# Performance work log

Measured on AMD Instinct MI355X. Metric: run time of the kernel, lower is better.

## Reference

```python
import jax, jax.numpy as jnp
import numpy as np

N_NODES = 50000
D_IN = 64
HID = 64
OUT = 64
NEG_SLOPE = 0.2


def setup_inputs() -> dict:
    key = jax.random.key(0)
    ks = jax.random.split(key, 16)
    s = 1.0 / np.sqrt(D_IN)
    inp = {
        "x": jax.random.normal(ks[0], (N_NODES, D_IN), dtype=jnp.float32),
        "edge_index": jax.random.randint(ks[1], (2, 1200000), 0, N_NODES, dtype=jnp.int64),
        # conv1 (GATConv, heads=1): separate src/dst projections + attention vectors + bias
        "W1_src": jax.random.uniform(ks[2], (D_IN, HID), jnp.float32, -s, s),
        "W1_dst": jax.random.uniform(ks[3], (D_IN, HID), jnp.float32, -s, s),
        "att1_src": jax.random.uniform(ks[4], (HID,), jnp.float32, -s, s),
        "att1_dst": jax.random.uniform(ks[5], (HID,), jnp.float32, -s, s),
        "b1": jnp.zeros((HID,), jnp.float32),
        # lin1 residual
        "Wl1": jax.random.uniform(ks[6], (D_IN, HID), jnp.float32, -s, s),
        "bl1": jnp.zeros((HID,), jnp.float32),
        # conv2
        "W2_src": jax.random.uniform(ks[7], (HID, OUT), jnp.float32, -s, s),
        "W2_dst": jax.random.uniform(ks[8], (HID, OUT), jnp.float32, -s, s),
        "att2_src": jax.random.uniform(ks[9], (OUT,), jnp.float32, -s, s),
        "att2_dst": jax.random.uniform(ks[10], (OUT,), jnp.float32, -s, s),
        "b2": jnp.zeros((OUT,), jnp.float32),
        # lin2 residual
        "Wl2": jax.random.uniform(ks[11], (HID, OUT), jnp.float32, -s, s),
        "bl2": jnp.zeros((OUT,), jnp.float32),
    }
    return inp


def _gat_conv(x, W_src, W_dst, att_src, att_dst, bias, src, dst, n_nodes):
    # project nodes: [N, C]
    h_src = x @ W_src
    h_dst = x @ W_dst
    # per-node attention logits: [N]
    a_src = h_src @ att_src
    a_dst = h_dst @ att_dst
    # per-edge score, leaky relu (slope 0.2)
    e = a_src[src] + a_dst[dst]  # [E]
    e = jnp.where(e >= 0, e, NEG_SLOPE * e)
    # segment softmax over incoming edges of each dst node
    seg_max = jax.lax.stop_gradient(
        jax.ops.segment_max(e, dst, num_segments=n_nodes))  # [N]
    w = jnp.exp(e - seg_max[dst])  # [E]
    seg_sum = jax.ops.segment_sum(w, dst, num_segments=n_nodes)  # [N]
    alpha = w / seg_sum[dst]  # [E]
    # weighted scatter-add of gathered src features
    msg = h_src[src] * alpha[:, None]  # [E, C]
    out = jax.ops.segment_sum(msg, dst, num_segments=n_nodes)  # [N, C]
    return out + bias


def reference(x, edge_index, W1_src, W1_dst, att1_src, att1_dst, b1, Wl1, bl1,
              W2_src, W2_dst, att2_src, att2_dst, b2, Wl2, bl2):
    src, dst = edge_index[0], edge_index[1]
    n = x.shape[0]
    h = _gat_conv(x, W1_src, W1_dst, att1_src, att1_dst, b1, src, dst, n)
    h = jax.nn.relu(h + x @ Wl1 + bl1)
    o = _gat_conv(h, W2_src, W2_dst, att2_src, att2_dst, b2, src, dst, n)
    o = jax.nn.relu(o + h @ Wl2 + bl2)
    return o
```

## Files before the change

kernel.cpp:

```cpp
#include <hip/hip_runtime.h>
#include <hip/hip_fp16.h>

#define NEG 0.2f
#define BSHIFT 9
#define BNODES 512
#define ECAP 14336

__device__ __forceinline__ void agg_core(
    int beg, int end, float ad, int lane, int g, int l,
    const int* __restrict__ ssrc, const float* __restrict__ asrc,
    const float2* __restrict__ h8,
    float& a0, float& a1, float& a2, float& a3, float& sumw) {
    a0 = a1 = a2 = a3 = sumw = 0.f;
    while (beg < end) {
        int nb = min(64, end - beg);
        int s_l = 0; float w_l = 0.f;
        if (lane < nb) {
            s_l = ssrc[beg + lane];
            float e = asrc[s_l] + ad;
            e = (e >= 0.f) ? e : NEG * e;
            w_l = __expf(e);
        }
        int i = 0;
        for (; i + 15 < nb; i += 16) {
            int iA = i + g, iB = i + 4 + g, iC = i + 8 + g, iD = i + 12 + g;
            int   sA = __shfl(s_l, iA, 64), sB = __shfl(s_l, iB, 64);
            int   sC = __shfl(s_l, iC, 64), sD = __shfl(s_l, iD, 64);
            float wA = __shfl(w_l, iA, 64), wB = __shfl(w_l, iB, 64);
            float wC = __shfl(w_l, iC, 64), wD = __shfl(w_l, iD, 64);
            float2 rA = h8[(size_t)sA * 16 + l];
            float2 rB = h8[(size_t)sB * 16 + l];
            float2 rC = h8[(size_t)sC * 16 + l];
            float2 rD = h8[(size_t)sD * 16 + l];
            float2 fA0 = __half22float2(((const __half2*)&rA)[0]);
            float2 fA1 = __half22float2(((const __half2*)&rA)[1]);
            float2 fB0 = __half22float2(((const __half2*)&rB)[0]);
            float2 fB1 = __half22float2(((const __half2*)&rB)[1]);
            float2 fC0 = __half22float2(((const __half2*)&rC)[0]);
            float2 fC1 = __half22float2(((const __half2*)&rC)[1]);
            float2 fD0 = __half22float2(((const __half2*)&rD)[0]);
            float2 fD1 = __half22float2(((const __half2*)&rD)[1]);
            sumw += (wA + wB) + (wC + wD);
            a0 += wA * fA0.x + wB * fB0.x + wC * fC0.x + wD * fD0.x;
            a1 += wA * fA0.y + wB * fB0.y + wC * fC0.y + wD * fD0.y;
            a2 += wA * fA1.x + wB * fB1.x + wC * fC1.x + wD * fD1.x;
            a3 += wA * fA1.y + wB * fB1.y + wC * fC1.y + wD * fD1.y;
        }
        for (; i + 7 < nb; i += 8) {
            int iA = i + g, iB = i + 4 + g;
            int   sA = __shfl(s_l, iA, 64), sB = __shfl(s_l, iB, 64);
            float wA = __shfl(w_l, iA, 64), wB = __shfl(w_l, iB, 64);
            float2 rA = h8[(size_t)sA * 16 + l];
            float2 rB = h8[(size_t)sB * 16 + l];
            float2 fA0 = __half22float2(((const __half2*)&rA)[0]);
            float2 fA1 = __half22float2(((const __half2*)&rA)[1]);
            float2 fB0 = __half22float2(((const __half2*)&rB)[0]);
            float2 fB1 = __half22float2(((const __half2*)&rB)[1]);
            sumw += wA + wB;
            a0 += wA * fA0.x + wB * fB0.x;
            a1 += wA * fA0.y + wB * fB0.y;
            a2 += wA * fA1.x + wB * fB1.x;
            a3 += wA * fA1.y + wB * fB1.y;
        }
        for (; i < nb; i += 4) {
            int iA = i + g;
            int   sA = __shfl(s_l, iA, 64);
            float wA = __shfl(w_l, iA, 64);
            float2 rA = h8[(size_t)sA * 16 + l];
            float2 fA0 = __half22float2(((const __half2*)&rA)[0]);
            float2 fA1 = __half22float2(((const __half2*)&rA)[1]);
            sumw += wA;
            a0 += wA * fA0.x; a1 += wA * fA0.y;
            a2 += wA * fA1.x; a3 += wA * fA1.y;
        }
        beg += nb;
    }
    a0 += __shfl_xor(a0, 16, 64); a0 += __shfl_xor(a0, 32, 64);
    a1 += __shfl_xor(a1, 16, 64); a1 += __shfl_xor(a1, 32, 64);
    a2 += __shfl_xor(a2, 16, 64); a2 += __shfl_xor(a2, 32, 64);
    a3 += __shfl_xor(a3, 16, 64); a3 += __shfl_xor(a3, 32, 64);
    sumw += __shfl_xor(sumw, 16, 64); sumw += __shfl_xor(sumw, 32, 64);
}

__global__ __launch_bounds__(256) void bin_prep(
    const int* __restrict__ src, const int* __restrict__ dst,
    int* __restrict__ gcur, unsigned* __restrict__ binned, int E, int K,
    const float* __restrict__ W1s, const float* __restrict__ a1s,
    const float* __restrict__ W1d, const float* __restrict__ a1d,
    const float* __restrict__ W2s, const float* __restrict__ a2s,
    const float* __restrict__ W2d, const float* __restrict__ a2d,
    float* __restrict__ vecs) {
    int t = threadIdx.x;
    if (blockIdx.x == gridDim.x - 1) {
        int g = t >> 6, k = t & 63;
        const float* W = (g == 0) ? W1s : (g == 1) ? W1d : (g == 2) ? W2s : W2d;
        const float* a = (g == 0) ? a1s : (g == 1) ? a1d : (g == 2) ? a2s : a2d;
        float s = 0.f;
        #pragma unroll 8
        for (int j = 0; j < 64; ++j) s += W[k * 64 + j] * a[j];
        vecs[t] = s;
        return;
    }
    __shared__ int h[128], cbase[128], cur[128];
    if (t < 128) h[t] = 0;
    __syncthreads();
    int base = blockIdx.x * 2048;
    #pragma unroll
    for (int i = 0; i < 8; ++i) {
        int idx = base + i * 256 + t;
        if (idx < E) atomicAdd(&h[dst[idx] >> BSHIFT], 1);
    }
    __syncthreads();
    if (t < K) {
        cbase[t] = t * ECAP + (h[t] ? atomicAdd(&gcur[t], h[t]) : 0);
        cur[t] = 0;
    }
    __syncthreads();
    #pragma unroll
    for (int i = 0; i < 8; ++i) {
        int idx = base + i * 256 + t;
        if (idx < E) {
            int d = dst[idx], s = src[idx];
            int b = d >> BSHIFT;
            int pos = cbase[b] + atomicAdd(&cur[b], 1);
            binned[pos] = ((unsigned)s << BSHIFT) | (unsigned)(d & (BNODES - 1));
        }
    }
}

__device__ __forceinline__ void gemm_tile(
    int tid, int row0, int rows,
    const __half* WsH, const __half* WlH, const float* xs,
    const float* bias_s, const float* vs_s, const float* vd_s,
    __half2* __restrict__ hsrc, float* __restrict__ base_out,
    float* __restrict__ asrc, float* __restrict__ adst) {
    int r0 = (tid >> 3) * 2;
    int cg = tid & 7, c0 = cg * 8;
    if (r0 >= rows) return;

    float a0[8], a1[8], b0[8], b1[8];
    #pragma unroll
    for (int i = 0; i < 8; ++i) { a0[i] = a1[i] = b0[i] = b1[i] = 0.f; }
    float as0 = 0.f, ad0 = 0.f, as1 = 0.f, ad1 = 0.f;

    #pragma unroll 8
    for (int k = 0; k < 64; ++k) {
        float xv0 = xs[r0 * 65 + k];
        float xv1 = xs[(r0 + 1) * 65 + k];
        float4 wsv = *(const float4*)&WsH[(k << 6) + c0];
        float4 wlv = *(const float4*)&WlH[(k << 6) + c0];
        const __half2* hs = (const __half2*)&wsv;
        const __half2* hl = (const __half2*)&wlv;
        #pragma unroll
        for (int p = 0; p < 4; ++p) {
            float2 w = __half22float2(hs[p]);
            a0[2*p]   += xv0 * w.x;  a0[2*p+1] += xv0 * w.y;
            a1[2*p]   += xv1 * w.x;  a1[2*p+1] += xv1 * w.y;
            float2 l = __half22float2(hl[p]);
            b0[2*p]   += xv0 * l.x;  b0[2*p+1] += xv0 * l.y;
            b1[2*p]   += xv1 * l.x;  b1[2*p+1] += xv1 * l.y;
        }
        float vsk = vs_s[k], vdk = vd_s[k];
        as0 += xv0 * vsk;  ad0 += xv0 * vdk;
        as1 += xv1 * vsk;  ad1 += xv1 * vdk;
    }

    int rg0 = row0 + r0, rg1 = rg0 + 1;
    bool row1ok = (r0 + 1) < rows;
    float4 pack;
    ((__half2*)&pack)[0] = __floats2half2_rn(a0[0], a0[1]);
    ((__half2*)&pack)[1] = __floats2half2_rn(a0[2], a0[3]);
    ((__half2*)&pack)[2] = __floats2half2_rn(a0[4], a0[5]);
    ((__half2*)&pack)[3] = __floats2half2_rn(a0[6], a0[7]);
    *(float4*)&hsrc[(size_t)rg0 * 32 + (c0 >> 1)] = pack;
    if (row1ok) {
        ((__half2*)&pack)[0] = __floats2half2_rn(a1[0], a1[1]);
        ((__half2*)&pack)[1] = __floats2half2_rn(a1[2], a1[3]);
        ((__half2*)&pack)[2] = __floats2half2_rn(a1[4], a1[5]);
        ((__half2*)&pack)[3] = __floats2half2_rn(a1[6], a1[7]);
        *(float4*)&hsrc[(size_t)rg1 * 32 + (c0 >> 1)] = pack;
    }
    float4 bA = *(const float4*)&bias_s[c0];
    float4 bB = *(const float4*)&bias_s[c0 + 4];
    float4 o;
    o.x = b0[0] + bA.x; o.y = b0[1] + bA.y; o.z = b0[2] + bA.z; o.w = b0[3] + bA.w;
    *(float4*)&base_out[(size_t)rg0 * 64 + c0] = o;
    o.x = b0[4] + bB.x; o.y = b0[5] + bB.y; o.z = b0[6] + bB.z; o.w = b0[7] + bB.w;
    *(float4*)&base_out[(size_t)rg0 * 64 + c0 + 4] = o;
    if (row1ok) {
        o.x = b1[0] + bA.x; o.y = b1[1] + bA.y; o.z = b1[2] + bA.z; o.w = b1[3] + bA.w;
        *(float4*)&base_out[(size_t)rg1 * 64 + c0] = o;
        o.x = b1[4] + bB.x; o.y = b1[5] + bB.y; o.z = b1[6] + bB.z; o.w = b1[7] + bB.w;
        *(float4*)&base_out[(size_t)rg1 * 64 + c0 + 4] = o;
    }
    if (cg == 0) {
        asrc[rg0] = as0; adst[rg0] = ad0;
        if (row1ok) { asrc[rg1] = as1; adst[rg1] = ad1; }
    }
}

__global__ __launch_bounds__(256) void csr_gemm(
    const unsigned* __restrict__ binned, int* __restrict__ ssrc,
    const int* __restrict__ gcur, int* __restrict__ rowbeg, int* __restrict__ rowend,
    const float* __restrict__ x, const float* __restrict__ Wsrc,
    const float* __restrict__ Wl, const float* __restrict__ vsrc,
    const float* __restrict__ vdst, const float* __restrict__ bconv,
    const float* __restrict__ blin,
    __half2* __restrict__ hsrc, float* __restrict__ base_out,
    float* __restrict__ asrc, float* __restrict__ adst, int N, int K) {
    __shared__ union {
        struct { __half WsH[4096]; __half WlH[4096]; float xs[64 * 65];
                 float bias[64]; float vs[64]; float vd[64]; } g;
        struct { int lh[BNODES]; int ps[256]; } c;
    } sm;
    int tid = threadIdx.x;
    int blk = blockIdx.x;

    if (blk < K) {
        int base = blk * ECAP;
        int cnt = min(gcur[blk], ECAP);
        sm.c.lh[tid] = 0; sm.c.lh[tid + 256] = 0;
        __syncthreads();
        for (int i = tid; i < cnt; i += 256)
            atomicAdd(&sm.c.lh[binned[base + i] & (BNODES - 1)], 1);
        __syncthreads();
        int a0 = sm.c.lh[2 * tid], a1 = sm.c.lh[2 * tid + 1];
        sm.c.ps[tid] = a0 + a1;
        __syncthreads();
        for (int off = 1; off < 256; off <<= 1) {
            int v = (tid >= off) ? sm.c.ps[tid - off] : 0;
            __syncthreads();
            sm.c.ps[tid] += v;
            __syncthreads();
        }
        int exc = sm.c.ps[tid] - (a0 + a1);
        int node0 = blk * BNODES + 2 * tid, node1 = node0 + 1;
        if (node0 < N) { rowbeg[node0] = base + exc;      rowend[node0] = base + exc + a0; }
        if (node1 < N) { rowbeg[node1] = base + exc + a0; rowend[node1] = base + exc + a0 + a1; }
        __syncthreads();
        sm.c.lh[2 * tid] = exc; sm.c.lh[2 * tid + 1] = exc + a0;
        __syncthreads();
        for (int i = tid; i < cnt; i += 256) {
            unsigned e = binned[base + i];
            int pos = atomicAdd(&sm.c.lh[e & (BNODES - 1)], 1);
            ssrc[base + pos] = (int)(e >> BSHIFT);
        }
        return;
    }

    int gb = blk - K;
    #pragma unroll
    for (int i = 0; i < 4; ++i) {
        int idx4 = tid * 4 + i * 1024;
        float4 ws = *(const float4*)&Wsrc[idx4];
        float4 wl = *(const float4*)&Wl[idx4];
        *(__half2*)&sm.g.WsH[idx4]     = __floats2half2_rn(ws.x, ws.y);
        *(__half2*)&sm.g.WsH[idx4 + 2] = __floats2half2_rn(ws.z, ws.w);
        *(__half2*)&sm.g.WlH[idx4]     = __floats2half2_rn(wl.x, wl.y);
        *(__half2*)&sm.g.WlH[idx4 + 2] = __floats2half2_rn(wl.z, wl.w);
    }
    if (tid < 64) {
        sm.g.bias[tid] = bconv[tid] + blin[tid];
        sm.g.vs[tid]   = vsrc[tid];
        sm.g.vd[tid]   = vdst[tid];
    }
    int row0 = gb * 64;
    int rows = min(64, N - row0);
    #pragma unroll
    for (int i = 0; i < 16; ++i) {
        int idx = tid + i * 256;
        int r = idx >> 6, cc = idx & 63;
        if (r < rows) sm.g.xs[r * 65 + cc] = x[(size_t)(row0 + r) * 64 + cc];
    }
    __syncthreads();
    gemm_tile(tid, row0, rows, sm.g.WsH, sm.g.WlH, sm.g.xs,
              sm.g.bias, sm.g.vs, sm.g.vd, hsrc, base_out, asrc, adst);
}

__global__ __launch_bounds__(256) void node_gemm_h(
    const __half2* __restrict__ xh, const float* __restrict__ Wsrc,
    const float* __restrict__ Wl, const float* __restrict__ vsrc,
    const float* __restrict__ vdst, const float* __restrict__ bconv,
    const float* __restrict__ blin,
    __half2* __restrict__ hsrc, float* __restrict__ base_out,
    float* __restrict__ asrc, float* __restrict__ adst, int n) {
    __shared__ __half WsH[4096];
    __shared__ __half WlH[4096];
    __shared__ float xs[64 * 65];
    __shared__ float bias_s[64], vs_s[64], vd_s[64];

    int tid = threadIdx.x;
    #pragma unroll
    for (int i = 0; i < 4; ++i) {
        int idx4 = tid * 4 + i * 1024;
        float4 ws = *(const float4*)&Wsrc[idx4];
        float4 wl = *(const float4*)&Wl[idx4];
        *(__half2*)&WsH[idx4]     = __floats2half2_rn(ws.x, ws.y);
        *(__half2*)&WsH[idx4 + 2] = __floats2half2_rn(ws.z, ws.w);
        *(__half2*)&WlH[idx4]     = __floats2half2_rn(wl.x, wl.y);
        *(__half2*)&WlH[idx4 + 2] = __floats2half2_rn(wl.z, wl.w);
    }
    if (tid < 64) {
        bias_s[tid] = bconv[tid] + blin[tid];
        vs_s[tid]   = vsrc[tid];
        vd_s[tid]   = vdst[tid];
    }
    int row0 = blockIdx.x * 64;
    int rows = min(64, n - row0);
    const float4* xf4 = (const float4*)xh;
    #pragma unroll
    for (int i = 0; i < 2; ++i) {
        int idx = tid + i * 256;
        int r = idx >> 3, cg8 = (idx & 7) * 8;
        if (r < rows) {
            float4 v = xf4[(size_t)(row0 + r) * 8 + (idx & 7)];
            const __half2* hv = (const __half2*)&v;
            float2 f0 = __half22float2(hv[0]);
            float2 f1 = __half22float2(hv[1]);
            float2 f2 = __half22float2(hv[2]);
            float2 f3 = __half22float2(hv[3]);
            float* dstp = &xs[r * 65 + cg8];
            dstp[0] = f0.x; dstp[1] = f0.y; dstp[2] = f1.x; dstp[3] = f1.y;
            dstp[4] = f2.x; dstp[5] = f2.y; dstp[6] = f3.x; dstp[7] = f3.y;
        }
    }
    __syncthreads();
    gemm_tile(tid, row0, rows, WsH, WlH, xs, bias_s, vs_s, vd_s,
              hsrc, base_out, asrc, adst);
}

__global__ __launch_bounds__(256) void gat_aggregate_h(
    const int* __restrict__ rowbeg, const int* __restrict__ rowend,
    const int* __restrict__ ssrc,
    const float* __restrict__ asrc, const float* __restrict__ adst,
    const float2* __restrict__ h8, const float* __restrict__ base,
    __half2* __restrict__ out, int N) {
    int d = blockIdx.x * 4 + (threadIdx.x >> 6);
    int lane = threadIdx.x & 63, g = lane >> 4, l = lane & 15;
    if (d >= N) return;
    float a0, a1, a2, a3, sw;
    agg_core(rowbeg[d], rowend[d], adst[d], lane, g, l, ssrc, asrc, h8,
             a0, a1, a2, a3, sw);
    if (g == 0) {
        float4 b4 = *(const float4*)&base[(size_t)d * 64 + 4 * l];
        float invw = (sw > 0.f) ? 1.f / sw : 0.f;
        float2 pk;
        ((__half2*)&pk)[0] = __floats2half2_rn(fmaxf(b4.x + a0 * invw, 0.f),
                                               fmaxf(b4.y + a1 * invw, 0.f));
        ((__half2*)&pk)[1] = __floats2half2_rn(fmaxf(b4.z + a2 * invw, 0.f),
                                               fmaxf(b4.w + a3 * invw, 0.f));
        *(float2*)&out[(size_t)d * 32 + 2 * l] = pk;
    }
}

__global__ __launch_bounds__(256) void gat_aggregate_f(
    const int* __restrict__ rowbeg, const int* __restrict__ rowend,
    const int* __restrict__ ssrc,
    const float* __restrict__ asrc, const float* __restrict__ adst,
    const float2* __restrict__ h8, const float* __restrict__ base,
    float* __restrict__ out, int N) {
    int d = blockIdx.x * 4 + (threadIdx.x >> 6);
    int lane = threadIdx.x & 63, g = lane >> 4, l = lane & 15;
    if (d >= N) return;
    float a0, a1, a2, a3, sw;
    agg_core(rowbeg[d], rowend[d], adst[d], lane, g, l, ssrc, asrc, h8,
             a0, a1, a2, a3, sw);
    if (g == 0) {
        float4 b4 = *(const float4*)&base[(size_t)d * 64 + 4 * l];
        float invw = (sw > 0.f) ? 1.f / sw : 0.f;
        float4 o;
        o.x = fmaxf(b4.x + a0 * invw, 0.f);
        o.y = fmaxf(b4.y + a1 * invw, 0.f);
        o.z = fmaxf(b4.z + a2 * invw, 0.f);
        o.w = fmaxf(b4.w + a3 * invw, 0.f);
        *(float4*)&out[(size_t)d * 64 + 4 * l] = o;
    }
}

extern "C" void kernel_launch(void* const* d_in, const int* in_sizes, int n_in,
                              void* d_out, int out_size, void* d_ws, size_t ws_size,
                              hipStream_t stream) {
    const float* x    = (const float*)d_in[0];
    const int*   ei   = (const int*)d_in[1];
    const float* W1s  = (const float*)d_in[2];
    const float* W1d  = (const float*)d_in[3];
    const float* a1s  = (const float*)d_in[4];
    const float* a1d  = (const float*)d_in[5];
    const float* b1   = (const float*)d_in[6];
    const float* Wl1  = (const float*)d_in[7];
    const float* bl1  = (const float*)d_in[8];
    const float* W2s  = (const float*)d_in[9];
    const float* W2d  = (const float*)d_in[10];
    const float* a2s  = (const float*)d_in[11];
    const float* a2d  = (const float*)d_in[12];
    const float* b2   = (const float*)d_in[13];
    const float* Wl2  = (const float*)d_in[14];
    const float* bl2  = (const float*)d_in[15];

    const int N = in_sizes[0] / 64;
    const int E = in_sizes[1] / 2;
    const int* src = ei;
    const int* dst = ei + E;
    const int K = (N + BNODES - 1) >> BSHIFT;

    float* ws = (float*)d_ws;
    size_t o = 0;
    __half2* hsrcH = (__half2*)(ws + o); o += (size_t)N * 32;
    __half2* hmidH = (__half2*)(ws + o); o += (size_t)N * 32;
    float* base   = ws + o; o += (size_t)N * 64;
    float* asrc   = ws + o; o += N;
    float* adst   = ws + o; o += N;
    float* vecs   = ws + o; o += 256;
    int* rowbeg = (int*)(ws + o); o += N;
    int* rowend = (int*)(ws + o); o += N;
    int* gcur   = (int*)(ws + o); o += 128;
    unsigned* binned = (unsigned*)(ws + o); o += (size_t)K * ECAP;
    int* ssrc   = (int*)(ws + o); o += (size_t)K * ECAP;

    const int EB = (E + 2047) / 2048;
    const int GB = (N + 63) / 64;

    (void)hipMemsetAsync(gcur, 0, 128 * sizeof(int), stream);
    bin_prep<<<EB + 1, 256, 0, stream>>>(src, dst, gcur, binned, E, K,
                                         W1s, a1s, W1d, a1d, W2s, a2s, W2d, a2d, vecs);

    csr_gemm<<<K + GB, 256, 0, stream>>>(
        binned, ssrc, gcur, rowbeg, rowend,
        x, W1s, Wl1, vecs, vecs + 64, b1, bl1,
        hsrcH, base, asrc, adst, N, K);

    gat_aggregate_h<<<(N + 3) / 4, 256, 0, stream>>>(
        rowbeg, rowend, ssrc, asrc, adst, (const float2*)hsrcH, base, hmidH, N);

    node_gemm_h<<<GB, 256, 0, stream>>>(hmidH, W2s, Wl2, vecs + 128, vecs + 192,
                                        b2, bl2, hsrcH, base, asrc, adst, N);

    gat_aggregate_f<<<(N + 3) / 4, 256, 0, stream>>>(
        rowbeg, rowend, ssrc, asrc, adst, (const float2*)hsrcH, base,
        (float*)d_out, N);
}
```

Measured before the change: 230.4 us.

## Use MFMA f16 for node projection GEMMs with prepacked fragment weights

```diff
diff --git a/kernel.cpp b/kernel.cpp
--- a/kernel.cpp
+++ b/kernel.cpp
@@ -5,6 +5,9 @@
 #define BSHIFT 9
 #define BNODES 512
 #define ECAP 14336
+
+typedef _Float16 half8_t __attribute__((ext_vector_type(8)));
+typedef float   floatx4_t __attribute__((ext_vector_type(4)));
 
 __device__ __forceinline__ void agg_core(
     int beg, int end, float ad, int lane, int g, int l,
@@ -89,16 +92,47 @@
     const float* __restrict__ W1d, const float* __restrict__ a1d,
     const float* __restrict__ W2s, const float* __restrict__ a2s,
     const float* __restrict__ W2d, const float* __restrict__ a2d,
-    float* __restrict__ vecs) {
+    const float* __restrict__ Wl1, const float* __restrict__ Wl2,
+    __half* __restrict__ wf) {
     int t = threadIdx.x;
     if (blockIdx.x == gridDim.x - 1) {
-        int g = t >> 6, k = t & 63;
-        const float* W = (g == 0) ? W1s : (g == 1) ? W1d : (g == 2) ? W2s : W2d;
-        const float* a = (g == 0) ? a1s : (g == 1) ? a1d : (g == 2) ? a2s : a2d;
-        float s = 0.f;
-        #pragma unroll 8
-        for (int j = 0; j < 64; ++j) s += W[k * 64 + j] * a[j];
-        vecs[t] = s;
+        __shared__ float vsm[256];
+        {
+            int g = t >> 6, k = t & 63;
+            const float* W = (g == 0) ? W1s : (g == 1) ? W1d : (g == 2) ? W2s : W2d;
+            const float* a = (g == 0) ? a1s : (g == 1) ? a1d : (g == 2) ? a2s : a2d;
+            float s = 0.f;
+            #pragma unroll 8
+            for (int j = 0; j < 64; ++j) s += W[k * 64 + j] * a[j];
+            vsm[t] = s;
+        }
+        __syncthreads();
+        __half* wS1 = wf;
+        __half* wL1 = wf + 4096;
+        __half* wV1 = wf + 8192;
+        __half* wS2 = wf + 9216;
+        __half* wL2 = wf + 13312;
+        __half* wV2 = wf + 17408;
+        for (int e = t; e < 4096; e += 256) {
+            int j = e & 7, ln = (e >> 3) & 63, tile = e >> 9;
+            int nt = tile >> 1, kt = tile & 1;
+            int kk = kt * 32 + ((ln >> 4) << 3) + j;
+            int nn = (nt << 4) + (ln & 15);
+            int wi = kk * 64 + nn;
+            wS1[e] = __float2half(W1s[wi]);
+            wL1[e] = __float2half(Wl1[wi]);
+            wS2[e] = __float2half(W2s[wi]);
+            wL2[e] = __float2half(Wl2[wi]);
+        }
+        for (int e = t; e < 1024; e += 256) {
+            int j = e & 7, ln = (e >> 3) & 63, kt = e >> 9;
+            int kk = kt * 32 + ((ln >> 4) << 3) + j;
+            int nn = ln & 15;
+            float v1 = (nn == 0) ? vsm[kk] : (nn == 1) ? vsm[64 + kk] : 0.f;
+            float v2 = (nn == 0) ? vsm[128 + kk] : (nn == 1) ? vsm[192 + kk] : 0.f;
+            wV1[e] = __float2half(v1);
+            wV2[e] = __float2half(v2);
+        }
         return;
     }
     __shared__ int h[128], cbase[128], cur[128];
@@ -128,90 +162,89 @@
     }
 }
 
-__device__ __forceinline__ void gemm_tile(
+__device__ __forceinline__ void mfma_tile(
     int tid, int row0, int rows,
-    const __half* WsH, const __half* WlH, const float* xs,
-    const float* bias_s, const float* vs_s, const float* vd_s,
+    _Float16* xh, float* xf,
+    const __half* wsF, const __half* wlF, const __half* wvF,
+    const float* __restrict__ bconv, const float* __restrict__ blin,
     __half2* __restrict__ hsrc, float* __restrict__ base_out,
     float* __restrict__ asrc, float* __restrict__ adst) {
-    int r0 = (tid >> 3) * 2;
-    int cg = tid & 7, c0 = cg * 8;
-    if (r0 >= rows) return;
-
-    float a0[8], a1[8], b0[8], b1[8];
-    #pragma unroll
-    for (int i = 0; i < 8; ++i) { a0[i] = a1[i] = b0[i] = b1[i] = 0.f; }
-    float as0 = 0.f, ad0 = 0.f, as1 = 0.f, ad1 = 0.f;
-
-    #pragma unroll 8
-    for (int k = 0; k < 64; ++k) {
-        float xv0 = xs[r0 * 65 + k];
-        float xv1 = xs[(r0 + 1) * 65 + k];
-        float4 wsv = *(const float4*)&WsH[(k << 6) + c0];
-        float4 wlv = *(const float4*)&WlH[(k << 6) + c0];
-        const __half2* hs = (const __half2*)&wsv;
-        const __half2* hl = (const __half2*)&wlv;
+    int w = tid >> 6, lane = tid & 63, m = lane & 15, q = lane >> 4;
+    half8_t a0 = *(const half8_t*)&xh[(w * 16 + m) * 72 + q * 8];
+    half8_t a1 = *(const half8_t*)&xh[(w * 16 + m) * 72 + 32 + q * 8];
+    const half8_t* bS = (const half8_t*)(const void*)wsF;
+    const half8_t* bL = (const half8_t*)(const void*)wlF;
+    const half8_t* bV = (const half8_t*)(const void*)wvF;
+    floatx4_t z = {0.f, 0.f, 0.f, 0.f};
+    floatx4_t cs[4], cl[4], cv;
+    #pragma unroll
+    for (int nt = 0; nt < 4; ++nt) {
+        cs[nt] = __builtin_amdgcn_mfma_f32_16x16x32_f16(a0, bS[(nt * 2 + 0) * 64 + lane], z, 0, 0, 0);
+        cs[nt] = __builtin_amdgcn_mfma_f32_16x16x32_f16(a1, bS[(nt * 2 + 1) * 64 + lane], cs[nt], 0, 0, 0);
+        cl[nt] = __builtin_amdgcn_mfma_f32_16x16x32_f16(a0, bL[(nt * 2 + 0) * 64 + lane], z, 0, 0, 0);
+        cl[nt] = __builtin_amdgcn_mfma_f32_16x16x32_f16(a1, bL[(nt * 2 + 1) * 64 + lane], cl[nt], 0, 0, 0);
+    }
+    cv = __builtin_amdgcn_mfma_f32_16x16x32_f16(a0, bV[lane], z, 0, 0, 0);
+    cv = __builtin_amdgcn_mfma_f32_16x16x32_f16(a1, bV[64 + lane], cv, 0, 0, 0);
+    __syncthreads();
+    #pragma unroll
+    for (int nt = 0; nt < 4; ++nt)
         #pragma unroll
-        for (int p = 0; p < 4; ++p) {
-            float2 w = __half22float2(hs[p]);
-            a0[2*p]   += xv0 * w.x;  a0[2*p+1] += xv0 * w.y;
-            a1[2*p]   += xv1 * w.x;  a1[2*p+1] += xv1 * w.y;
-            float2 l = __half22float2(hl[p]);
-            b0[2*p]   += xv0 * l.x;  b0[2*p+1] += xv0 * l.y;
-            b1[2*p]   += xv1 * l.x;  b1[2*p+1] += xv1 * l.y;
-        }
-        float vsk = vs_s[k], vdk = vd_s[k];
-        as0 += xv0 * vsk;  ad0 += xv0 * vdk;
-        as1 += xv1 * vsk;  ad1 += xv1 * vdk;
-    }
-
-    int rg0 = row0 + r0, rg1 = rg0 + 1;
-    bool row1ok = (r0 + 1) < rows;
-    float4 pack;
-    ((__half2*)&pack)[0] = __floats2half2_rn(a0[0], a0[1]);
-    ((__half2*)&pack)[1] = __floats2half2_rn(a0[2], a0[3]);
-    ((__half2*)&pack)[2] = __floats2half2_rn(a0[4], a0[5]);
-    ((__half2*)&pack)[3] = __floats2half2_rn(a0[6], a0[7]);
-    *(float4*)&hsrc[(size_t)rg0 * 32 + (c0 >> 1)] = pack;
-    if (row1ok) {
-        ((__half2*)&pack)[0] = __floats2half2_rn(a1[0], a1[1]);
-        ((__half2*)&pack)[1] = __floats2half2_rn(a1[2], a1[3]);
-        ((__half2*)&pack)[2] = __floats2half2_rn(a1[4], a1[5]);
-        ((__half2*)&pack)[3] = __floats2half2_rn(a1[6], a1[7]);
-        *(float4*)&hsrc[(size_t)rg1 * 32 + (c0 >> 1)] = pack;
-    }
-    float4 bA = *(const float4*)&bias_s[c0];
-    float4 bB = *(const float4*)&bias_s[c0 + 4];
-    float4 o;
-    o.x = b0[0] + bA.x; o.y = b0[1] + bA.y; o.z = b0[2] + bA.z; o.w = b0[3] + bA.w;
-    *(float4*)&base_out[(size_t)rg0 * 64 + c0] = o;
-    o.x = b0[4] + bB.x; o.y = b0[5] + bB.y; o.z = b0[6] + bB.z; o.w = b0[7] + bB.w;
-    *(float4*)&base_out[(size_t)rg0 * 64 + c0 + 4] = o;
-    if (row1ok) {
-        o.x = b1[0] + bA.x; o.y = b1[1] + bA.y; o.z = b1[2] + bA.z; o.w = b1[3] + bA.w;
-        *(float4*)&base_out[(size_t)rg1 * 64 + c0] = o;
-        o.x = b1[4] + bB.x; o.y = b1[5] + bB.y; o.z = b1[6] + bB.z; o.w = b1[7] + bB.w;
-        *(float4*)&base_out[(size_t)rg1 * 64 + c0 + 4] = o;
-    }
-    if (cg == 0) {
-        asrc[rg0] = as0; adst[rg0] = ad0;
-        if (row1ok) { asrc[rg1] = as1; adst[rg1] = ad1; }
+        for (int r = 0; r < 4; ++r)
+            xh[(w * 16 + q * 4 + r) * 72 + nt * 16 + m] = (_Float16)cs[nt][r];
+    __syncthreads();
+    #pragma unroll
+    for (int i = 0; i < 2; ++i) {
+        int u = tid + i * 256;
+        int r = u >> 3, c8 = (u & 7) * 8;
+        if (r < rows) {
+            float4 v = *(const float4*)&xh[r * 72 + c8];
+            *(float4*)&hsrc[(size_t)(row0 + r) * 32 + (u & 7) * 4] = v;
+        }
+    }
+    __syncthreads();
+    float bb[4];
+    bb[0] = bconv[m] + blin[m];
+    bb[1] = bconv[16 + m] + blin[16 + m];
+    bb[2] = bconv[32 + m] + blin[32 + m];
+    bb[3] = bconv[48 + m] + blin[48 + m];
+    #pragma unroll
+    for (int nt = 0; nt < 4; ++nt)
+        #pragma unroll
+        for (int r = 0; r < 4; ++r)
+            xf[(w * 16 + q * 4 + r) * 68 + nt * 16 + m] = cl[nt][r] + bb[nt];
+    __syncthreads();
+    #pragma unroll
+    for (int i = 0; i < 4; ++i) {
+        int u = tid + i * 256;
+        int r = u >> 4, c4 = (u & 15) * 4;
+        if (r < rows)
+            *(float4*)&base_out[(size_t)(row0 + r) * 64 + c4] = *(const float4*)&xf[r * 68 + c4];
+    }
+    int rb = w * 16 + q * 4;
+    if (m == 0) {
+        #pragma unroll
+        for (int r = 0; r < 4; ++r)
+            if (rb + r < rows) asrc[row0 + rb + r] = cv[r];
+    } else if (m == 1) {
+        #pragma unroll
+        for (int r = 0; r < 4; ++r)
+            if (rb + r < rows) adst[row0 + rb + r] = cv[r];
     }
 }
 
 __global__ __launch_bounds__(256) void csr_gemm(
     const unsigned* __restrict__ binned, int* __restrict__ ssrc,
     const int* __restrict__ gcur, int* __restrict__ rowbeg, int* __restrict__ rowend,
-    const float* __restrict__ x, const float* __restrict__ Wsrc,
-    const float* __restrict__ Wl, const float* __restrict__ vsrc,
-    const float* __restrict__ vdst, const float* __restrict__ bconv,
-    const float* __restrict__ blin,
+    const float* __restrict__ x, const __half* __restrict__ wsF,
+    const __half* __restrict__ wlF, const __half* __restrict__ wvF,
+    const float* __restrict__ bconv, const float* __restrict__ blin,
     __half2* __restrict__ hsrc, float* __restrict__ base_out,
     float* __restrict__ asrc, float* __restrict__ adst, int N, int K) {
     __shared__ union {
-        struct { __half WsH[4096]; __half WlH[4096]; float xs[64 * 65];
-                 float bias[64]; float vs[64]; float vd[64]; } g;
-        struct { int lh[BNODES]; int ps[256]; } c;
+        struct { int lh[512]; int ps[256]; } c;
+        _Float16 xh[64 * 72];
+        float    xf[64 * 68];
     } sm;
     int tid = threadIdx.x;
     int blk = blockIdx.x;
@@ -249,84 +282,47 @@
     }
 
     int gb = blk - K;
-    #pragma unroll
-    for (int i = 0; i < 4; ++i) {
-        int idx4 = tid * 4 + i * 1024;
-        float4 ws = *(const float4*)&Wsrc[idx4];
-        float4 wl = *(const float4*)&Wl[idx4];
-        *(__half2*)&sm.g.WsH[idx4]     = __floats2half2_rn(ws.x, ws.y);
-        *(__half2*)&sm.g.WsH[idx4 + 2] = __floats2half2_rn(ws.z, ws.w);
-        *(__half2*)&sm.g.WlH[idx4]     = __floats2half2_rn(wl.x, wl.y);
-        *(__half2*)&sm.g.WlH[idx4 + 2] = __floats2half2_rn(wl.z, wl.w);
-    }
-    if (tid < 64) {
-        sm.g.bias[tid] = bconv[tid] + blin[tid];
-        sm.g.vs[tid]   = vsrc[tid];
-        sm.g.vd[tid]   = vdst[tid];
-    }
     int row0 = gb * 64;
     int rows = min(64, N - row0);
     #pragma unroll
-    for (int i = 0; i < 16; ++i) {
-        int idx = tid + i * 256;
-        int r = idx >> 6, cc = idx & 63;
-        if (r < rows) sm.g.xs[r * 65 + cc] = x[(size_t)(row0 + r) * 64 + cc];
-    }
-    __syncthreads();
-    gemm_tile(tid, row0, rows, sm.g.WsH, sm.g.WlH, sm.g.xs,
-              sm.g.bias, sm.g.vs, sm.g.vd, hsrc, base_out, asrc, adst);
-}
-
-__global__ __launch_bounds__(256) void node_gemm_h(
-    const __half2* __restrict__ xh, const float* __restrict__ Wsrc,
-    const float* __restrict__ Wl, const float* __restrict__ vsrc,
-    const float* __restrict__ vdst, const float* __restrict__ bconv,
-    const float* __restrict__ blin,
+    for (int i = 0; i < 4; ++i) {
+        int u = tid + i * 256;
+        int r = u >> 4, c4 = (u & 15) * 4;
+        if (r < rows) {
+            float4 v = *(const float4*)&x[(size_t)(row0 + r) * 64 + c4];
+            *(__half2*)&sm.xh[r * 72 + c4]     = __floats2half2_rn(v.x, v.y);
+            *(__half2*)&sm.xh[r * 72 + c4 + 2] = __floats2half2_rn(v.z, v.w);
+        }
+    }
+    __syncthreads();
+    mfma_tile(tid, row0, rows, sm.xh, sm.xf, wsF, wlF, wvF,
+              bconv, blin, hsrc, base_out, asrc, adst);
+}
+
+__global__ __launch_bounds__(256) void node_gemm2(
+    const __half* __restrict__ xh_in, const __half* __restrict__ wsF,
+    const __half* __restrict__ wlF, const __half* __restrict__ wvF,
+    const float* __restrict__ bconv, const float* __restrict__ blin,
     __half2* __restrict__ hsrc, float* __restrict__ base_out,
-    float* __restrict__ asrc, float* __restrict__ adst, int n) {
-    __shared__ __half WsH[4096];
-    __shared__ __half WlH[4096];
-    __shared__ float xs[64 * 65];
-    __shared__ float bias_s[64], vs_s[64], vd_s[64];
-
+    float* __restrict__ asrc, float* __restrict__ adst, int N) {
+    __shared__ union {
+        _Float16 xh[64 * 72];
+        float    xf[64 * 68];
+    } sm;
     int tid = threadIdx.x;
-    #pragma unroll
-    for (int i = 0; i < 4; ++i) {
-        int idx4 = tid * 4 + i * 1024;
-        float4 ws = *(const float4*)&Wsrc[idx4];
-        float4 wl = *(const float4*)&Wl[idx4];
-        *(__half2*)&WsH[idx4]     = __floats2half2_rn(ws.x, ws.y);
-        *(__half2*)&WsH[idx4 + 2] = __floats2half2_rn(ws.z, ws.w);
-        *(__half2*)&WlH[idx4]     = __floats2half2_rn(wl.x, wl.y);
-        *(__half2*)&WlH[idx4 + 2] = __floats2half2_rn(wl.z, wl.w);
-    }
-    if (tid < 64) {
-        bias_s[tid] = bconv[tid] + blin[tid];
-        vs_s[tid]   = vsrc[tid];
-        vd_s[tid]   = vdst[tid];
-    }
     int row0 = blockIdx.x * 64;
-    int rows = min(64, n - row0);
-    const float4* xf4 = (const float4*)xh;
+    int rows = min(64, N - row0);
     #pragma unroll
     for (int i = 0; i < 2; ++i) {
-        int idx = tid + i * 256;
-        int r = idx >> 3, cg8 = (idx & 7) * 8;
-        if (r < rows) {
-            float4 v = xf4[(size_t)(row0 + r) * 8 + (idx & 7)];
-            const __half2* hv = (const __half2*)&v;
-            float2 f0 = __half22float2(hv[0]);
-            float2 f1 = __half22float2(hv[1]);
-            float2 f2 = __half22float2(hv[2]);
-            float2 f3 = __half22float2(hv[3]);
-            float* dstp = &xs[r * 65 + cg8];
-            dstp[0] = f0.x; dstp[1] = f0.y; dstp[2] = f1.x; dstp[3] = f1.y;
-            dstp[4] = f2.x; dstp[5] = f2.y; dstp[6] = f3.x; dstp[7] = f3.y;
-        }
-    }
-    __syncthreads();
-    gemm_tile(tid, row0, rows, WsH, WlH, xs, bias_s, vs_s, vd_s,
-              hsrc, base_out, asrc, adst);
+        int u = tid + i * 256;
+        int r = u >> 3, c8 = (u & 7) * 8;
+        if (r < rows)
+            *(float4*)&sm.xh[r * 72 + c8] =
+                *(const float4*)&xh_in[(size_t)(row0 + r) * 64 + c8];
+    }
+    __syncthreads();
+    mfma_tile(tid, row0, rows, sm.xh, sm.xf, wsF, wlF, wvF,
+              bconv, blin, hsrc, base_out, asrc, adst);
 }
 
 __global__ __launch_bounds__(256) void gat_aggregate_h(
@@ -410,30 +406,38 @@
     float* base   = ws + o; o += (size_t)N * 64;
     float* asrc   = ws + o; o += N;
     float* adst   = ws + o; o += N;
-    float* vecs   = ws + o; o += 256;
+    __half* wf    = (__half*)(ws + o); o += 9216;
     int* rowbeg = (int*)(ws + o); o += N;
     int* rowend = (int*)(ws + o); o += N;
     int* gcur   = (int*)(ws + o); o += 128;
     unsigned* binned = (unsigned*)(ws + o); o += (size_t)K * ECAP;
     int* ssrc   = (int*)(ws + o); o += (size_t)K * ECAP;
 
+    const __half* wS1 = wf;
+    const __half* wL1 = wf + 4096;
+    const __half* wV1 = wf + 8192;
+    const __half* wS2 = wf + 9216;
+    const __half* wL2 = wf + 13312;
+    const __half* wV2 = wf + 17408;
+
     const int EB = (E + 2047) / 2048;
     const int GB = (N + 63) / 64;
 
     (void)hipMemsetAsync(gcur, 0, 128 * sizeof(int), stream);
     bin_prep<<<EB + 1, 256, 0, stream>>>(src, dst, gcur, binned, E, K,
-                                         W1s, a1s, W1d, a1d, W2s, a2s, W2d, a2d, vecs);
+                                         W1s, a1s, W1d, a1d, W2s, a2s, W2d, a2d,
+                                         Wl1, Wl2, wf);
 
     csr_gemm<<<K + GB, 256, 0, stream>>>(
         binned, ssrc, gcur, rowbeg, rowend,
-        x, W1s, Wl1, vecs, vecs + 64, b1, bl1,
+        x, wS1, wL1, wV1, b1, bl1,
         hsrcH, base, asrc, adst, N, K);
 
     gat_aggregate_h<<<(N + 3) / 4, 256, 0, stream>>>(
         rowbeg, rowend, ssrc, asrc, adst, (const float2*)hsrcH, base, hmidH, N);
 
-    node_gemm_h<<<GB, 256, 0, stream>>>(hmidH, W2s, Wl2, vecs + 128, vecs + 192,
-                                        b2, bl2, hsrcH, base, asrc, adst, N);
+    node_gemm2<<<GB, 256, 0, stream>>>((const __half*)hmidH, wS2, wL2, wV2,
+                                       b2, bl2, hsrcH, base, asrc, adst, N);
 
     gat_aggregate_f<<<(N + 3) / 4, 256, 0, stream>>>(
         rowbeg, rowend, ssrc, asrc, adst, (const float2*)hsrcH, base,
```

Result: faster. 213.9 us (-7.1%).
